# Kernel optimization log

Measured on AMD Instinct MI355X. Metric: run time of the kernel, lower is better.

Reference implementation:

```python
import jax, jax.numpy as jnp
from jax import lax
import numpy as np

W_DIM = 512
B, CIN, COUT, H = 16, 128, 128, 128
KS = 3
UP, DOWN = 2, 2
TAPS = 12
GAIN = float(np.sqrt(2.0))
SLOPE = 0.2
CLAMP = 256.0
# gauss_spline(0, n=1) = 1/sqrt(2*pi*(n+1)/12); zero_filter = sqrt(f*f) = f at alpha=1
ZF = float(1.0 / np.sqrt(2.0 * np.pi / 6.0))


def _lowpass(numtaps, cutoff, fs, beta=8.0):
    # Kaiser-windowed sinc lowpass, normalized to unit DC gain (stands in for design_lowpass_filter)
    n = np.arange(numtaps) - (numtaps - 1) / 2.0
    h = np.sinc(2.0 * cutoff / fs * n) * np.kaiser(numtaps, beta)
    return jnp.asarray((h / h.sum()).astype(np.float32))


def setup_inputs() -> dict:
    key = jax.random.key(0)
    ks = jax.random.split(key, 6)
    fs_tmp = 128 * UP  # tmp_sampling_rate = max(in_sr,out_sr)*lrelu_upsampling
    return {
        "x": jax.random.normal(ks[0], (B, CIN, H, H), jnp.float32),
        "w": jax.random.normal(ks[1], (B, W_DIM), jnp.float32),
        "affine_weight": jax.random.normal(ks[2], (CIN, W_DIM), jnp.float32),
        "affine_bias": jnp.ones((CIN,), jnp.float32),  # bias_init=1
        "kernel_weight": jax.random.normal(ks[3], (COUT, CIN, KS, KS), jnp.float32),
        "bias": jnp.zeros((COUT,), jnp.float32),
        "up_filter": _lowpass(TAPS, 64.0, fs_tmp),
        "down_filter": _lowpass(TAPS, 64.0, fs_tmp),
        "magnitude_ema": jnp.ones((), jnp.float32),
    }


def reference(x, w, affine_weight, affine_bias, kernel_weight, bias, up_filter, down_filter, magnitude_ema):
    # --- affine (FullyConnectedLayer, linear): weight_gain = 1/sqrt(in_features) ---
    s = w @ (affine_weight.T * (1.0 / np.sqrt(W_DIM))) + affine_bias  # [B, CIN]

    # --- SynthesisGroupKernel: kernel = test_weight * zero_filter * gain(ks); gain=1, zf const ---
    wk = kernel_weight * ZF  # [COUT, CIN, 3, 3]

    # --- modulated_conv2d (demodulate=True) ---
    wk = wk * lax.rsqrt(jnp.mean(wk * wk, axis=(1, 2, 3), keepdims=True))
    s = s * lax.rsqrt(jnp.mean(s * s))
    ww = wk[None] * s[:, None, :, None, None]                      # [B, COUT, CIN, 3, 3]
    dcoefs = lax.rsqrt(jnp.sum(ww * ww, axis=(2, 3, 4)) + 1e-8)    # [B, COUT]
    ww = ww * dcoefs[:, :, None, None, None]
    ww = ww * (magnitude_ema ** -0.5)                              # input_gain = ema.rsqrt()
    xg = x.reshape(1, B * CIN, H, H)
    wg = ww.reshape(B * COUT, CIN, KS, KS)
    y = lax.conv_general_dilated(xg, wg, (1, 1), [(1, 1), (1, 1)], feature_group_count=B)
    y = y.reshape(B, COUT, H, H)

    # --- filtered_lrelu: FIR upsample x2, bias + lrelu + gain + clamp, FIR downsample x2 ---
    fu2 = jnp.outer(up_filter, up_filter) * (UP * UP)              # up gain folded into filter
    fd2 = jnp.outer(down_filter, down_filter)
    wu = jnp.broadcast_to(fu2, (COUT, 1, TAPS, TAPS))
    wd = jnp.broadcast_to(fd2, (COUT, 1, TAPS, TAPS))
    # upsample: zero-stuff via lhs_dilation; 128 -> 256
    y = lax.conv_general_dilated(y, wu, (1, 1), [(6, 6), (6, 6)], lhs_dilation=(UP, UP),
                                 feature_group_count=COUT)
    y = y + bias[None, :, None, None]
    y = jnp.where(y >= 0, y, y * SLOPE) * GAIN
    y = jnp.clip(y, -CLAMP, CLAMP)
    # downsample: FIR + stride 2; 256 -> 128
    y = lax.conv_general_dilated(y, wd, (DOWN, DOWN), [(5, 5), (5, 5)], feature_group_count=COUT)
    return y
```

## Files before the change

kernel.cpp:

```cpp
#include <hip/hip_runtime.h>

typedef unsigned short ushort_t;
typedef __attribute__((ext_vector_type(8))) short bf16x8;
typedef __attribute__((ext_vector_type(4))) float f32x4;
typedef __attribute__((ext_vector_type(4))) unsigned int u32x4;

#define ZF 0.9770840884556017f
#define SQ2 1.4142135623730951f

__device__ __forceinline__ ushort_t f2bf(float f) {
    unsigned u = __float_as_uint(f);
    unsigned r = (u + 0x7fffu + ((u >> 16) & 1u)) >> 16;
    return (ushort_t)r;
}
__device__ __forceinline__ float bf2f(ushort_t h) {
    return __uint_as_float(((unsigned)h) << 16);
}

__global__ void kzero(float* ssum) { if (threadIdx.x == 0) ssum[0] = 0.f; }

__global__ __launch_bounds__(128) void ks(const float* __restrict__ w,
                                          const float* __restrict__ aw,
                                          const float* __restrict__ ab,
                                          float* sbuf, float* ssum) {
    int b = blockIdx.x, c = threadIdx.x;
    const float4* wp = (const float4*)(w + b * 512);
    const float4* ap = (const float4*)(aw + c * 512);
    float acc = 0.f;
    for (int k = 0; k < 128; ++k) {
        float4 xv = wp[k], yv = ap[k];
        acc += xv.x * yv.x + xv.y * yv.y + xv.z * yv.z + xv.w * yv.w;
    }
    float s = acc * 0.04419417382415922f + ab[c];
    sbuf[b * 128 + c] = s;
    float sq = s * s;
#pragma unroll
    for (int m = 1; m < 64; m <<= 1) sq += __shfl_xor(sq, m);
    if ((c & 63) == 0) atomicAdd(ssum, sq);
}

__global__ __launch_bounds__(128) void kkn(const float* __restrict__ kw,
                                           const float* __restrict__ ssum,
                                           float* kn, float* srstd) {
    int o = blockIdx.x, t = threadIdx.x;
    float acc = 0.f;
    for (int j = t; j < 1152; j += 128) { float v = kw[o * 1152 + j] * ZF; acc += v * v; }
#pragma unroll
    for (int m = 1; m < 64; m <<= 1) acc += __shfl_xor(acc, m);
    __shared__ float red[2];
    if ((t & 63) == 0) red[t >> 6] = acc;
    __syncthreads();
    if (t == 0) {
        kn[o] = ZF * rsqrtf((red[0] + red[1]) * (1.0f / 1152.0f));
        if (o == 0) srstd[0] = rsqrtf(ssum[0] * (1.0f / 2048.0f));
    }
}

__global__ __launch_bounds__(128) void kww(const float* __restrict__ kw,
                                           const float* __restrict__ sbuf,
                                           const float* __restrict__ kn,
                                           const float* __restrict__ srstd,
                                           const float* __restrict__ ema,
                                           ushort_t* __restrict__ wwbf) {
    int o = blockIdx.x, b = blockIdx.y, i = threadIdx.x;
    float sn = sbuf[b * 128 + i] * srstd[0];
    float knv = kn[o];
    const float* kwp = kw + (o * 128 + i) * 9;
    float wv[9];
    float ssq = 0.f;
#pragma unroll
    for (int t = 0; t < 9; ++t) { float v = kwp[t] * knv * sn; wv[t] = v; ssq += v * v; }
#pragma unroll
    for (int m = 1; m < 64; m <<= 1) ssq += __shfl_xor(ssq, m);
    __shared__ float red[2];
    if ((i & 63) == 0) red[i >> 6] = ssq;
    __syncthreads();
    float tot = red[0] + red[1];
    float g = rsqrtf(tot + 1e-8f) * rsqrtf(ema[0]);
#pragma unroll
    for (int t = 0; t < 9; ++t)
        wwbf[((size_t)(b * 128 + o)) * 1152 + t * 128 + i] = f2bf(wv[t] * g);
}

__global__ __launch_bounds__(256) void kT(const float* __restrict__ x, ushort_t* __restrict__ xT) {
    int h = blockIdx.x, b = blockIdx.y;
    __shared__ ushort_t tile[128 * 132];
    int tid = threadIdx.x;
    const float* xb = x + (size_t)b * 2097152 + (size_t)h * 128;
#pragma unroll 4
    for (int it = 0; it < 16; ++it) {
        int idx = it * 256 + tid;
        int cin = idx >> 5, c4 = idx & 31;
        float4 v = *(const float4*)(xb + (size_t)cin * 16384 + c4 * 4);
        union { ushort_t us[4]; unsigned long long u; } p;
        p.us[0] = f2bf(v.x); p.us[1] = f2bf(v.y); p.us[2] = f2bf(v.z); p.us[3] = f2bf(v.w);
        *(unsigned long long*)(tile + cin * 132 + c4 * 4) = p.u;
    }
    __syncthreads();
    ushort_t* ob = xT + ((size_t)(b * 128 + h)) * 16384;
#pragma unroll 2
    for (int it = 0; it < 8; ++it) {
        int idx = it * 256 + tid;
        int wcol = idx >> 4;
        int cinb = (idx & 15) << 3;
        union { ushort_t us[8]; u32x4 v; } p;
#pragma unroll
        for (int j = 0; j < 8; ++j) p.us[j] = tile[(cinb + j) * 132 + wcol];
        *(u32x4*)(ob + (size_t)wcol * 128 + cinb) = p.v;
    }
}

__global__ __launch_bounds__(256) void kC(const ushort_t* __restrict__ xT,
                                          const ushort_t* __restrict__ wwbf,
                                          ushort_t* __restrict__ ybf) {
    const int b = blockIdx.y;
    const int tile = blockIdx.x;
    const int R0 = (tile >> 3) * 4;
    const int C0 = (tile & 7) * 16;
    const int tid = threadIdx.x;
    const int wid = tid >> 6;
    const int lane = tid & 63;
    const int lr = lane & 15;
    const int lg = lane >> 4;

    __shared__ __align__(16) unsigned char xs[6 * 18 * 128 * 2];

    const ushort_t* xTb = xT + (size_t)b * 2097152;
    for (int q = tid; q < 1728; q += 256) {
        int cinb = (q & 15) << 3;
        int rc = q >> 4;
        int row = rc / 18;
        int col = rc - row * 18;
        int gr = R0 - 1 + row, gc = C0 - 1 + col;
        u32x4 v = {0u, 0u, 0u, 0u};
        if ((unsigned)gr < 128u && (unsigned)gc < 128u)
            v = *(const u32x4*)(xTb + (((size_t)(gr << 7) + gc) << 7) + cinb);
        int byte = ((row * 18 + col) << 8) + (cinb << 1);
        byte ^= (col & 7) << 4;
        *(u32x4*)(xs + byte) = v;
    }
    __syncthreads();

    const ushort_t* wwp = wwbf + ((size_t)(b * 128 + wid * 32)) * 1152;
    f32x4 acc[2][4] = {};
#pragma unroll
    for (int tap = 0; tap < 9; ++tap) {
        const int dr = tap / 3, dc = tap - dr * 3;
#pragma unroll
        for (int kq = 0; kq < 4; ++kq) {
            const int kloc = kq * 32 + lg * 8;
            const int kglob = tap * 128 + kloc;
            bf16x8 a0 = *(const bf16x8*)(wwp + lr * 1152 + kglob);
            bf16x8 a1 = *(const bf16x8*)(wwp + (lr + 16) * 1152 + kglob);
#pragma unroll
            for (int nf = 0; nf < 4; ++nf) {
                int col = lr + dc;
                int byte = (((nf + dr) * 18 + col) << 8) + (kloc << 1);
                byte ^= (col & 7) << 4;
                bf16x8 bfr = *(const bf16x8*)(xs + byte);
                acc[0][nf] = __builtin_amdgcn_mfma_f32_16x16x32_bf16(a0, bfr, acc[0][nf], 0, 0, 0);
                acc[1][nf] = __builtin_amdgcn_mfma_f32_16x16x32_bf16(a1, bfr, acc[1][nf], 0, 0, 0);
            }
        }
    }

    ushort_t* yb = ybf + (size_t)b * 2097152;
#pragma unroll
    for (int mf = 0; mf < 2; ++mf)
#pragma unroll
        for (int nf = 0; nf < 4; ++nf)
#pragma unroll
            for (int r = 0; r < 4; ++r) {
                int cout = wid * 32 + mf * 16 + lg * 4 + r;
                int row = R0 + nf, colp = C0 + lr;
                yb[(((size_t)cout << 7) + row) * 128 + colp] = f2bf(acc[mf][nf][r]);
            }
}

__global__ __launch_bounds__(256) void kF(const ushort_t* __restrict__ ybf,
                                          const float* __restrict__ bias,
                                          const float* __restrict__ upf,
                                          const float* __restrict__ dnf,
                                          float* __restrict__ out) {
    int tileid = blockIdx.x, co = blockIdx.y, b = blockIdx.z;
    int R0 = (tileid >> 2) * 32, C0 = (tileid & 3) * 32;
    int tid = threadIdx.x;
    __shared__ float A[74 * 76];
    __shared__ float Bm[42 * 76];

    float fue[6], fuo[6], fre[6], fro[6], fd[12];
#pragma unroll
    for (int m = 0; m < 6; ++m) {
        float e = 2.0f * upf[2 * m], o = 2.0f * upf[2 * m + 1];
        fue[m] = e; fuo[m] = o;
        fre[m] = SQ2 * e; fro[m] = SQ2 * o;
    }
#pragma unroll
    for (int j = 0; j < 12; ++j) fd[j] = dnf[j];
    float bv = SQ2 * bias[co];

    const ushort_t* ych = ybf + ((size_t)(b * 128 + co) << 14);
    int yr0 = R0 - 5, yc0 = C0 - 5;
    for (int idx = tid; idx < 1764; idx += 256) {
        int r = idx / 42, c = idx - r * 42;
        int gr = yr0 + r, gc = yc0 + c;
        float v = 0.f;
        if ((unsigned)gr < 128u && (unsigned)gc < 128u) v = bf2f(ych[(gr << 7) + gc]);
        A[r * 44 + c] = v;
    }
    __syncthreads();
    for (int it = tid; it < 42 * 37; it += 256) {
        int r = it / 37, k = it - r * 37;
        const float* yr = A + r * 44 + k;
        float y0 = yr[0], y1 = yr[1], y2 = yr[2], y3 = yr[3], y4 = yr[4], y5 = yr[5];
        float s0 = fuo[0] * y0 + fuo[1] * y1 + fuo[2] * y2 + fuo[3] * y3 + fuo[4] * y4 + fuo[5] * y5;
        float s1 = fue[0] * y0 + fue[1] * y1 + fue[2] * y2 + fue[3] * y3 + fue[4] * y4 + fue[5] * y5;
        float* bp = Bm + r * 76 + 2 * k;
        bp[0] = s0; bp[1] = s1;
    }
    __syncthreads();
    int U0r = 2 * R0 - 5, U0c = 2 * C0 - 5;
    for (int it = tid; it < 37 * 74; it += 256) {
        int kr = it / 74, uc = it - kr * 74;
        const float* bc = Bm + kr * 76 + uc;
        float b0 = bc[0], b1 = bc[76], b2 = bc[152], b3 = bc[228], b4 = bc[304], b5 = bc[380];
        float t0 = bv + fro[0] * b0 + fro[1] * b1 + fro[2] * b2 + fro[3] * b3 + fro[4] * b4 + fro[5] * b5;
        float t1 = bv + fre[0] * b0 + fre[1] * b1 + fre[2] * b2 + fre[3] * b3 + fre[4] * b4 + fre[5] * b5;
        t0 = fmaxf(t0, 0.f) + 0.2f * fminf(t0, 0.f);
        t1 = fmaxf(t1, 0.f) + 0.2f * fminf(t1, 0.f);
        t0 = fminf(fmaxf(t0, -256.f), 256.f);
        t1 = fminf(fmaxf(t1, -256.f), 256.f);
        bool cv = (unsigned)(U0c + uc) < 256u;
        int gur = U0r + 2 * kr;
        bool rv0 = cv && ((unsigned)gur < 256u);
        bool rv1 = cv && ((unsigned)(gur + 1) < 256u);
        float* zp = A + 2 * kr * 76 + uc;
        zp[0]  = rv0 ? t0 : 0.f;
        zp[76] = rv1 ? t1 : 0.f;
    }
    __syncthreads();
    for (int it = tid; it < 74 * 8; it += 256) {
        int ur = it >> 3, q = it & 7;
        const float* z = A + ur * 76 + 8 * q;
        float win[18];
#pragma unroll
        for (int j = 0; j < 18; ++j) win[j] = z[j];
        float* dp = Bm + ur * 33 + 4 * q;
#pragma unroll
        for (int i = 0; i < 4; ++i) {
            float s = 0.f;
#pragma unroll
            for (int j = 0; j < 12; ++j) s += fd[j] * win[2 * i + j];
            dp[i] = s;
        }
    }
    __syncthreads();
    {
        int qr = tid >> 5, oc = tid & 31;
        const float* d = Bm + (8 * qr) * 33 + oc;
        float win[18];
#pragma unroll
        for (int j = 0; j < 18; ++j) win[j] = d[j * 33];
        float* ob = out + (((size_t)(b * 128 + co) << 7) + R0) * 128 + C0 + oc;
#pragma unroll
        for (int i = 0; i < 4; ++i) {
            float s = 0.f;
#pragma unroll
            for (int j = 0; j < 12; ++j) s += fd[j] * win[2 * i + j];
            ob[(4 * qr + i) * 128] = s;
        }
    }
}

extern "C" void kernel_launch(void* const* d_in, const int* in_sizes, int n_in,
                              void* d_out, int out_size, void* d_ws, size_t ws_size,
                              hipStream_t stream) {
    const float* x    = (const float*)d_in[0];
    const float* w    = (const float*)d_in[1];
    const float* aw   = (const float*)d_in[2];
    const float* ab   = (const float*)d_in[3];
    const float* kw   = (const float*)d_in[4];
    const float* bias = (const float*)d_in[5];
    const float* upf  = (const float*)d_in[6];
    const float* dnf  = (const float*)d_in[7];
    const float* ema  = (const float*)d_in[8];
    float* out = (float*)d_out;
    char* ws = (char*)d_ws;

    float* sbuf  = (float*)ws;
    float* ssum  = (float*)(ws + 8192);
    float* srstd = (float*)(ws + 8196);
    float* kn    = (float*)(ws + 8448);
    ushort_t* wwbf = (ushort_t*)(ws + 16384);
    ushort_t* xT   = (ushort_t*)(ws + ((size_t)5 << 20));
    ushort_t* ybf  = (ushort_t*)(ws + ((size_t)5 << 20) + ((size_t)64 << 20));

    kzero<<<1, 64, 0, stream>>>(ssum);
    ks<<<16, 128, 0, stream>>>(w, aw, ab, sbuf, ssum);
    kkn<<<128, 128, 0, stream>>>(kw, ssum, kn, srstd);
    kww<<<dim3(128, 16), 128, 0, stream>>>(kw, sbuf, kn, srstd, ema, wwbf);
    kT<<<dim3(128, 16), 256, 0, stream>>>(x, xT);
    kC<<<dim3(256, 16), 256, 0, stream>>>(xT, wwbf, ybf);
    kF<<<dim3(16, 128, 16), 256, 0, stream>>>(ybf, bias, upf, dnf, out);
}
```

Baseline: 654.9 us.

## Double conv tile height and vectorize filtered-lrelu LDS passes with edge-only zeroing

The conv kernel now computes 8 output rows per block instead of 4. That halves the grid and reuses each loaded weight fragment across twice as many MFMAs, at the cost of a larger LDS halo tile, 64 accumulator registers and a non-unrolled tap loop. The filtered-lrelu kernel now does the vertical upsample pass on column pairs with float2 LDS reads. It drops per-element bounds masking and instead zeroes border strips only for edge tiles, and reads the downsample window with float4 loads using a padded stride of 77. Because the stride is odd, those float4 LDS reads are not 16-byte aligned, which risks slow or misaligned accesses.

```diff
diff --git a/kernel.cpp b/kernel.cpp
--- a/kernel.cpp
+++ b/kernel.cpp
@@ -115,7 +115,7 @@
                                           ushort_t* __restrict__ ybf) {
     const int b = blockIdx.y;
     const int tile = blockIdx.x;
-    const int R0 = (tile >> 3) * 4;
+    const int R0 = (tile >> 3) * 8;
     const int C0 = (tile & 7) * 16;
     const int tid = threadIdx.x;
     const int wid = tid >> 6;
@@ -123,10 +123,10 @@
     const int lr = lane & 15;
     const int lg = lane >> 4;
 
-    __shared__ __align__(16) unsigned char xs[6 * 18 * 128 * 2];
+    __shared__ __align__(16) unsigned char xs[10 * 18 * 128 * 2];
 
     const ushort_t* xTb = xT + (size_t)b * 2097152;
-    for (int q = tid; q < 1728; q += 256) {
+    for (int q = tid; q < 2880; q += 256) {
         int cinb = (q & 15) << 3;
         int rc = q >> 4;
         int row = rc / 18;
@@ -135,15 +135,15 @@
         u32x4 v = {0u, 0u, 0u, 0u};
         if ((unsigned)gr < 128u && (unsigned)gc < 128u)
             v = *(const u32x4*)(xTb + (((size_t)(gr << 7) + gc) << 7) + cinb);
-        int byte = ((row * 18 + col) << 8) + (cinb << 1);
+        int byte = (rc << 8) + (cinb << 1);
         byte ^= (col & 7) << 4;
         *(u32x4*)(xs + byte) = v;
     }
     __syncthreads();
 
     const ushort_t* wwp = wwbf + ((size_t)(b * 128 + wid * 32)) * 1152;
-    f32x4 acc[2][4] = {};
-#pragma unroll
+    f32x4 acc[2][8] = {};
+#pragma unroll 1
     for (int tap = 0; tap < 9; ++tap) {
         const int dr = tap / 3, dc = tap - dr * 3;
 #pragma unroll
@@ -153,7 +153,7 @@
             bf16x8 a0 = *(const bf16x8*)(wwp + lr * 1152 + kglob);
             bf16x8 a1 = *(const bf16x8*)(wwp + (lr + 16) * 1152 + kglob);
 #pragma unroll
-            for (int nf = 0; nf < 4; ++nf) {
+            for (int nf = 0; nf < 8; ++nf) {
                 int col = lr + dc;
                 int byte = (((nf + dr) * 18 + col) << 8) + (kloc << 1);
                 byte ^= (col & 7) << 4;
@@ -168,7 +168,7 @@
 #pragma unroll
     for (int mf = 0; mf < 2; ++mf)
 #pragma unroll
-        for (int nf = 0; nf < 4; ++nf)
+        for (int nf = 0; nf < 8; ++nf)
 #pragma unroll
             for (int r = 0; r < 4; ++r) {
                 int cout = wid * 32 + mf * 16 + lg * 4 + r;
@@ -185,7 +185,7 @@
     int tileid = blockIdx.x, co = blockIdx.y, b = blockIdx.z;
     int R0 = (tileid >> 2) * 32, C0 = (tileid & 3) * 32;
     int tid = threadIdx.x;
-    __shared__ float A[74 * 76];
+    __shared__ float A[74 * 77];
     __shared__ float Bm[42 * 76];
 
     float fue[6], fuo[6], fre[6], fro[6], fd[12];
@@ -215,36 +215,64 @@
         float y0 = yr[0], y1 = yr[1], y2 = yr[2], y3 = yr[3], y4 = yr[4], y5 = yr[5];
         float s0 = fuo[0] * y0 + fuo[1] * y1 + fuo[2] * y2 + fuo[3] * y3 + fuo[4] * y4 + fuo[5] * y5;
         float s1 = fue[0] * y0 + fue[1] * y1 + fue[2] * y2 + fue[3] * y3 + fue[4] * y4 + fue[5] * y5;
-        float* bp = Bm + r * 76 + 2 * k;
-        bp[0] = s0; bp[1] = s1;
-    }
-    __syncthreads();
-    int U0r = 2 * R0 - 5, U0c = 2 * C0 - 5;
-    for (int it = tid; it < 37 * 74; it += 256) {
-        int kr = it / 74, uc = it - kr * 74;
-        const float* bc = Bm + kr * 76 + uc;
-        float b0 = bc[0], b1 = bc[76], b2 = bc[152], b3 = bc[228], b4 = bc[304], b5 = bc[380];
-        float t0 = bv + fro[0] * b0 + fro[1] * b1 + fro[2] * b2 + fro[3] * b3 + fro[4] * b4 + fro[5] * b5;
-        float t1 = bv + fre[0] * b0 + fre[1] * b1 + fre[2] * b2 + fre[3] * b3 + fre[4] * b4 + fre[5] * b5;
-        t0 = fmaxf(t0, 0.f) + 0.2f * fminf(t0, 0.f);
-        t1 = fmaxf(t1, 0.f) + 0.2f * fminf(t1, 0.f);
-        t0 = fminf(fmaxf(t0, -256.f), 256.f);
-        t1 = fminf(fmaxf(t1, -256.f), 256.f);
-        bool cv = (unsigned)(U0c + uc) < 256u;
-        int gur = U0r + 2 * kr;
-        bool rv0 = cv && ((unsigned)gur < 256u);
-        bool rv1 = cv && ((unsigned)(gur + 1) < 256u);
-        float* zp = A + 2 * kr * 76 + uc;
-        zp[0]  = rv0 ? t0 : 0.f;
-        zp[76] = rv1 ? t1 : 0.f;
-    }
-    __syncthreads();
+        float2 sv; sv.x = s0; sv.y = s1;
+        *(float2*)(Bm + r * 76 + 2 * k) = sv;
+    }
+    __syncthreads();
+    for (int it = tid; it < 37 * 37; it += 256) {
+        int kr = it / 37, jc = it - kr * 37;
+        const float* bc = Bm + kr * 76 + 2 * jc;
+        float2 c0 = *(const float2*)(bc);
+        float2 c1 = *(const float2*)(bc + 76);
+        float2 c2 = *(const float2*)(bc + 152);
+        float2 c3 = *(const float2*)(bc + 228);
+        float2 c4 = *(const float2*)(bc + 304);
+        float2 c5 = *(const float2*)(bc + 380);
+        float t00 = bv + fro[0] * c0.x + fro[1] * c1.x + fro[2] * c2.x + fro[3] * c3.x + fro[4] * c4.x + fro[5] * c5.x;
+        float t01 = bv + fro[0] * c0.y + fro[1] * c1.y + fro[2] * c2.y + fro[3] * c3.y + fro[4] * c4.y + fro[5] * c5.y;
+        float t10 = bv + fre[0] * c0.x + fre[1] * c1.x + fre[2] * c2.x + fre[3] * c3.x + fre[4] * c4.x + fre[5] * c5.x;
+        float t11 = bv + fre[0] * c0.y + fre[1] * c1.y + fre[2] * c2.y + fre[3] * c3.y + fre[4] * c4.y + fre[5] * c5.y;
+        t00 = fmaxf(t00, 0.f) + 0.2f * fminf(t00, 0.f);
+        t01 = fmaxf(t01, 0.f) + 0.2f * fminf(t01, 0.f);
+        t10 = fmaxf(t10, 0.f) + 0.2f * fminf(t10, 0.f);
+        t11 = fmaxf(t11, 0.f) + 0.2f * fminf(t11, 0.f);
+        t00 = fminf(fmaxf(t00, -256.f), 256.f);
+        t01 = fminf(fmaxf(t01, -256.f), 256.f);
+        t10 = fminf(fmaxf(t10, -256.f), 256.f);
+        t11 = fminf(fmaxf(t11, -256.f), 256.f);
+        float* zp = A + (2 * kr) * 77 + 2 * jc;
+        zp[0] = t00; zp[1] = t01;
+        zp[77] = t10; zp[78] = t11;
+    }
+    __syncthreads();
+    {
+        bool tz = (R0 == 0), bz = (R0 == 96), lz = (C0 == 0), rz = (C0 == 96);
+        if (tz || bz) {
+            for (int idx = tid; idx < 370; idx += 256) {
+                int s = idx / 74, c = idx - s * 74;
+                if (tz) A[s * 77 + c] = 0.f;
+                if (bz) A[(69 + s) * 77 + c] = 0.f;
+            }
+        }
+        if (lz || rz) {
+            for (int idx = tid; idx < 370; idx += 256) {
+                int r = idx / 5, s = idx - r * 5;
+                if (lz) A[r * 77 + s] = 0.f;
+                if (rz) A[r * 77 + 69 + s] = 0.f;
+            }
+        }
+        if (tz || bz || lz || rz) __syncthreads();
+    }
     for (int it = tid; it < 74 * 8; it += 256) {
         int ur = it >> 3, q = it & 7;
-        const float* z = A + ur * 76 + 8 * q;
-        float win[18];
-#pragma unroll
-        for (int j = 0; j < 18; ++j) win[j] = z[j];
+        const float* z = A + ur * 77 + 8 * q;
+        float4 w0 = *(const float4*)(z);
+        float4 w1 = *(const float4*)(z + 4);
+        float4 w2 = *(const float4*)(z + 8);
+        float4 w3 = *(const float4*)(z + 12);
+        float2 w4 = *(const float2*)(z + 16);
+        float win[18] = {w0.x, w0.y, w0.z, w0.w, w1.x, w1.y, w1.z, w1.w,
+                         w2.x, w2.y, w2.z, w2.w, w3.x, w3.y, w3.z, w3.w, w4.x, w4.y};
         float* dp = Bm + ur * 33 + 4 * q;
 #pragma unroll
         for (int i = 0; i < 4; ++i) {
@@ -300,6 +328,6 @@
     kkn<<<128, 128, 0, stream>>>(kw, ssum, kn, srstd);
     kww<<<dim3(128, 16), 128, 0, stream>>>(kw, sbuf, kn, srstd, ema, wwbf);
     kT<<<dim3(128, 16), 256, 0, stream>>>(x, xT);
-    kC<<<dim3(256, 16), 256, 0, stream>>>(xT, wwbf, ybf);
+    kC<<<dim3(128, 16), 256, 0, stream>>>(xT, wwbf, ybf);
     kF<<<dim3(16, 128, 16), 256, 0, stream>>>(ybf, bias, upf, dnf, out);
 }
```

Measured after the change: 838.0 us. +28.0%, slower.
